# Kernel tuning notes

Measured on AMD Instinct MI355X. Metric: run time of the kernel, lower is better.

The kernel has to match this reference:

```python
import jax, jax.numpy as jnp
import numpy as np

N_SRC = 200000   # source (input) nodes
N_DST = 50000    # destination (output) nodes; dst node i == src node i (block convention)
E = 800000       # edges
IN = 256
OUT = 64
H = 3
SLOPE = 0.2      # leaky_relu negative_slope


def setup_inputs() -> dict:
    key = jax.random.key(0)
    k0, k1, k2, k3, k4, k5 = jax.random.split(key, 6)
    x = jax.random.normal(k0, (N_SRC, IN), dtype=jnp.float32)
    W = jax.random.normal(k1, (H * OUT, IN), dtype=jnp.float32) * (1.0 / np.sqrt(IN))
    attn_l = jax.random.normal(k2, (1, H, OUT), dtype=jnp.float32) * 0.1
    attn_r = jax.random.normal(k3, (1, H, OUT), dtype=jnp.float32) * 0.1
    src = jax.random.randint(k4, (E,), 0, N_SRC, dtype=jnp.int32)
    dst = jnp.sort(jax.random.randint(k5, (E,), 0, N_DST, dtype=jnp.int32))
    return {"x": x, "W": W, "attn_l": attn_l, "attn_r": attn_r, "src": src, "dst": dst}


def reference(x, W, attn_l, attn_r, src, dst):
    # fc + reshape to heads: [N_src, H, F]
    feat = (x @ W.T).reshape(N_SRC, H, OUT)
    # per-head attention logits
    el = jnp.sum(feat * attn_l, axis=-1)          # [N_src, H]
    er = jnp.sum(feat[:N_DST] * attn_r, axis=-1)  # [N_dst, H] (self_gather of out nodes)
    # edge scores: apply_edge + leaky_relu -> [E, H]
    e = jax.nn.leaky_relu(el[src] + er[dst], negative_slope=SLOPE)
    # segmented max over incoming edges of each dst node (gather_local_max)
    m = jax.ops.segment_max(e, dst, num_segments=N_DST)
    m = jnp.where(jnp.isfinite(m), m, jnp.float32(0))  # empty segments -> 0
    m = jax.lax.stop_gradient(m)
    ex = jnp.exp(e - m[dst])                       # [E, H]
    s = jax.ops.segment_sum(ex, dst, num_segments=N_DST)  # [N_dst, H]
    s = jnp.where(s == 0, jnp.float32(1), s)       # sum_exponent[sum==0] = 1
    att = ex / s[dst]                              # [E, H]
    # attention_gather: sum over edges of att * src feature -> [N_dst, H, F]
    out = jax.ops.segment_sum(att[:, :, None] * feat[src], dst, num_segments=N_DST)
    return out.reshape(N_DST, H * OUT)
```

## Files before the change

### kernel.cpp

```cpp
#include <hip/hip_runtime.h>
#include <hip/hip_bf16.h>

#define N_SRCN 200000
#define N_DSTN 50000
#define NEDGE 800000
#define KIN 256
#define NF 192
#define SLOPE 0.2f

typedef __attribute__((ext_vector_type(8))) short bf16x8;
typedef __attribute__((ext_vector_type(4))) float f32x4;

__device__ __forceinline__ unsigned short f2bf(float f) {
    union { float f; unsigned int u; } v; v.f = f;
    unsigned int u = v.u;
    return (unsigned short)((u + 0x7FFFu + ((u >> 16) & 1u)) >> 16);
}
__device__ __forceinline__ float bf2f(unsigned short h) {
    union { unsigned int u; float f; } v; v.u = ((unsigned int)h) << 16;
    return v.f;
}
__device__ __forceinline__ unsigned int cvt2(float lo, float hi) {
    __hip_bfloat162 h = __float22bfloat162_rn(float2{lo, hi});
    union { __hip_bfloat162 h; unsigned int u; } c; c.h = h;
    return c.u;
}

__global__ void prep_kernel(const float* __restrict__ W, unsigned short* __restrict__ Wp,
                            const int* __restrict__ dst, int* __restrict__ rp) {
    const int bid = blockIdx.x;
    if (bid < 24) {
        int tid = bid * 256 + threadIdx.x;
        if (tid >= 12 * 8 * 64) return;
        int lane = tid & 63;
        int g = tid >> 6;
        int nt = g % 12, ks = g / 12;
        int col = nt * 16 + (lane & 15);
        int k = ks * 32 + (lane >> 4) * 8;
        const float* wsrc = &W[col * KIN + k];
        unsigned short* o = &Wp[tid * 8];
        #pragma unroll
        for (int j = 0; j < 8; ++j) o[j] = f2bf(wsrc[j]);
    } else {
        int d = (bid - 24) * 256 + threadIdx.x;
        if (d > N_DSTN) return;
        int lo = 0, hi = NEDGE;
        while (lo < hi) {
            int mid = (lo + hi) >> 1;
            if (dst[mid] < d) lo = mid + 1; else hi = mid;
        }
        rp[d] = lo;
    }
}

__launch_bounds__(64, 4)
__global__ void gemm_feat(const float* __restrict__ x, const unsigned short* __restrict__ Wp,
                          const float* __restrict__ attn_l, const float* __restrict__ attn_r,
                          unsigned short* __restrict__ feat,
                          float* __restrict__ el, float* __restrict__ er) {
    const int lane = threadIdx.x;
    const int al = lane & 15, ah = lane >> 4;
    const int r0 = blockIdx.x * 16;

    const float* xrow = &x[(size_t)(r0 + al) * KIN + ah * 8];

    f32x4 acc[12] = {};
    float4 c0 = *(const float4*)&xrow[0];
    float4 c1 = *(const float4*)&xrow[4];

    #pragma unroll
    for (int ks = 0; ks < 8; ++ks) {
        float4 n0, n1;
        if (ks < 7) {
            n0 = *(const float4*)&xrow[(ks + 1) * 32];
            n1 = *(const float4*)&xrow[(ks + 1) * 32 + 4];
        }
        union { bf16x8 v; unsigned int u[4]; } av;
        av.u[0] = cvt2(c0.x, c0.y);
        av.u[1] = cvt2(c0.z, c0.w);
        av.u[2] = cvt2(c1.x, c1.y);
        av.u[3] = cvt2(c1.z, c1.w);
        const unsigned short* wbase = &Wp[(size_t)(ks * 12) * 512 + lane * 8];
        #pragma unroll
        for (int nt = 0; nt < 12; ++nt) {
            bf16x8 bv = *(const bf16x8*)&wbase[nt * 512];
            acc[nt] = __builtin_amdgcn_mfma_f32_16x16x32_bf16(av.v, bv, acc[nt], 0, 0, 0);
        }
        if (ks < 7) { c0 = n0; c1 = n1; }
    }

    #pragma unroll
    for (int nt = 0; nt < 12; ++nt) {
        const int col = nt * 16 + al;
        #pragma unroll
        for (int e = 0; e < 4; ++e) {
            const int row = r0 + ah * 4 + e;
            feat[(size_t)row * NF + col] = f2bf(acc[nt][e]);
        }
    }

    float Al[12], Ar[12];
    #pragma unroll
    for (int nt = 0; nt < 12; ++nt) {
        Al[nt] = attn_l[nt * 16 + al];
        Ar[nt] = attn_r[nt * 16 + al];
    }
    #pragma unroll
    for (int h = 0; h < 3; ++h) {
        #pragma unroll
        for (int e = 0; e < 4; ++e) {
            float sl = 0.f, sr = 0.f;
            #pragma unroll
            for (int q = 0; q < 4; ++q) {
                const int nt = h * 4 + q;
                sl += acc[nt][e] * Al[nt];
                sr += acc[nt][e] * Ar[nt];
            }
            #pragma unroll
            for (int m = 1; m <= 8; m <<= 1) {
                sl += __shfl_xor(sl, m);
                sr += __shfl_xor(sr, m);
            }
            if (al == 0) {
                const int row = r0 + ah * 4 + e;
                el[row * 3 + h] = sl;
                if (row < N_DSTN) er[row * 3 + h] = sr;
            }
        }
    }
}

__launch_bounds__(256)
__global__ void gather_kernel(const unsigned short* __restrict__ feat,
                              const float* __restrict__ el, const float* __restrict__ er,
                              const int* __restrict__ src, const int* __restrict__ rp,
                              float* __restrict__ out) {
    const int lane = threadIdx.x & 63;
    const int d = (blockIdx.x * blockDim.x + threadIdx.x) >> 6;
    if (d >= N_DSTN) return;
    const int lo = rp[d], hi = rp[d + 1];
    const float er0 = er[d * 3 + 0], er1 = er[d * 3 + 1], er2 = er[d * 3 + 2];

    float a0 = 0.f, a1 = 0.f, a2 = 0.f, s0 = 0.f, s1 = 0.f, s2 = 0.f;
    for (int base = lo; base < hi; base += 64) {
        const int cnt = min(64, hi - base);
        int sv = 0; float w0 = 0.f, w1 = 0.f, w2 = 0.f;
        if (lane < cnt) {
            sv = src[base + lane];
            float e0 = el[sv * 3 + 0] + er0; e0 = e0 >= 0.f ? e0 : SLOPE * e0; w0 = __expf(e0);
            float e1 = el[sv * 3 + 1] + er1; e1 = e1 >= 0.f ? e1 : SLOPE * e1; w1 = __expf(e1);
            float e2 = el[sv * 3 + 2] + er2; e2 = e2 >= 0.f ? e2 : SLOPE * e2; w2 = __expf(e2);
        }
        int j = 0;
        for (; j + 8 <= cnt; j += 8) {
            unsigned short f0[8], f1[8], f2[8];
            float u0[8], u1[8], u2[8];
            #pragma unroll
            for (int q = 0; q < 8; ++q) {
                const int sj = __shfl(sv, j + q);
                const unsigned short* fp = &feat[(size_t)sj * NF + lane];
                f0[q] = fp[0]; f1[q] = fp[64]; f2[q] = fp[128];
                u0[q] = __shfl(w0, j + q);
                u1[q] = __shfl(w1, j + q);
                u2[q] = __shfl(w2, j + q);
            }
            #pragma unroll
            for (int q = 0; q < 8; ++q) {
                s0 += u0[q]; a0 += u0[q] * bf2f(f0[q]);
                s1 += u1[q]; a1 += u1[q] * bf2f(f1[q]);
                s2 += u2[q]; a2 += u2[q] * bf2f(f2[q]);
            }
        }
        for (; j < cnt; ++j) {
            const int sj = __shfl(sv, j);
            const float u0 = __shfl(w0, j);
            const float u1 = __shfl(w1, j);
            const float u2 = __shfl(w2, j);
            const unsigned short* fp = &feat[(size_t)sj * NF + lane];
            s0 += u0; a0 += u0 * bf2f(fp[0]);
            s1 += u1; a1 += u1 * bf2f(fp[64]);
            s2 += u2; a2 += u2 * bf2f(fp[128]);
        }
    }
    if (hi == lo) { s0 = 1.f; s1 = 1.f; s2 = 1.f; }
    float* op = &out[(size_t)d * NF];
    op[lane]       = a0 / s0;
    op[64 + lane]  = a1 / s1;
    op[128 + lane] = a2 / s2;
}

extern "C" void kernel_launch(void* const* d_in, const int* in_sizes, int n_in,
                              void* d_out, int out_size, void* d_ws, size_t ws_size,
                              hipStream_t stream) {
    const float* x      = (const float*)d_in[0];
    const float* W      = (const float*)d_in[1];
    const float* attn_l = (const float*)d_in[2];
    const float* attn_r = (const float*)d_in[3];
    const int*   src    = (const int*)d_in[4];
    const int*   dst    = (const int*)d_in[5];
    float* out = (float*)d_out;

    char* ws = (char*)d_ws;
    unsigned short* feat = (unsigned short*)ws;
    float* el = (float*)(ws + 76800000);
    float* er = (float*)(ws + 79200000);
    unsigned short* Wp = (unsigned short*)(ws + 79800000);
    int*   rp = (int*)(ws + 79898304);

    prep_kernel<<<24 + 196, 256, 0, stream>>>(W, Wp, dst, rp);
    gemm_feat<<<12500, 64, 0, stream>>>(x, Wp, attn_l, attn_r, feat, el, er);
    gather_kernel<<<12500, 256, 0, stream>>>(feat, el, er, src, rp, out);
}
```

Before: 180.1 us.

## Make GEMM persistent with LDS-staged weights and pad el/er to float4

The feature GEMM becomes a persistent kernel of 256 blocks of 8 waves. Each block loads the packed bf16 weight matrix into LDS once with direct global-to-LDS loads, then loops over 16-row tiles, so the weights are no longer re-read from global memory for every tile. The el/er logits are stored with a stride of 4 floats so the gather kernel can fetch them with a single float4 load. In exchange, the software prefetch of x across k-steps is dropped, occupancy is limited to one 512-thread block per CU, and the el/er buffers become larger.

```diff
diff --git a/kernel.cpp b/kernel.cpp
--- a/kernel.cpp
+++ b/kernel.cpp
@@ -7,6 +7,8 @@
 #define KIN 256
 #define NF 192
 #define SLOPE 0.2f
+#define TILES16 12500
+#define NWAVES 2048
 
 typedef __attribute__((ext_vector_type(8))) short bf16x8;
 typedef __attribute__((ext_vector_type(4))) float f32x4;
@@ -24,6 +26,11 @@
     __hip_bfloat162 h = __float22bfloat162_rn(float2{lo, hi});
     union { __hip_bfloat162 h; unsigned int u; } c; c.h = h;
     return c.u;
+}
+__device__ __forceinline__ void gl_lds16(const void* g, void* l) {
+    __builtin_amdgcn_global_load_lds(
+        (const __attribute__((address_space(1))) unsigned int*)g,
+        (__attribute__((address_space(3))) unsigned int*)l, 16, 0, 0);
 }
 
 __global__ void prep_kernel(const float* __restrict__ W, unsigned short* __restrict__ Wp,
@@ -53,51 +60,23 @@
     }
 }
 
-__launch_bounds__(64, 4)
-__global__ void gemm_feat(const float* __restrict__ x, const unsigned short* __restrict__ Wp,
-                          const float* __restrict__ attn_l, const float* __restrict__ attn_r,
-                          unsigned short* __restrict__ feat,
-                          float* __restrict__ el, float* __restrict__ er) {
-    const int lane = threadIdx.x;
+__global__ void __launch_bounds__(512, 1)
+gemm_feat(const float* __restrict__ x, const unsigned short* __restrict__ Wp,
+          const float* __restrict__ attn_l, const float* __restrict__ attn_r,
+          unsigned short* __restrict__ feat,
+          float* __restrict__ el4, float* __restrict__ er4) {
+    __shared__ unsigned short Bl[12 * 8 * 512];
+    const int t = threadIdx.x;
+    const int wid = t >> 6, lane = t & 63;
     const int al = lane & 15, ah = lane >> 4;
-    const int r0 = blockIdx.x * 16;
-
-    const float* xrow = &x[(size_t)(r0 + al) * KIN + ah * 8];
-
-    f32x4 acc[12] = {};
-    float4 c0 = *(const float4*)&xrow[0];
-    float4 c1 = *(const float4*)&xrow[4];
 
     #pragma unroll
-    for (int ks = 0; ks < 8; ++ks) {
-        float4 n0, n1;
-        if (ks < 7) {
-            n0 = *(const float4*)&xrow[(ks + 1) * 32];
-            n1 = *(const float4*)&xrow[(ks + 1) * 32 + 4];
-        }
-        union { bf16x8 v; unsigned int u[4]; } av;
-        av.u[0] = cvt2(c0.x, c0.y);
-        av.u[1] = cvt2(c0.z, c0.w);
-        av.u[2] = cvt2(c1.x, c1.y);
-        av.u[3] = cvt2(c1.z, c1.w);
-        const unsigned short* wbase = &Wp[(size_t)(ks * 12) * 512 + lane * 8];
-        #pragma unroll
-        for (int nt = 0; nt < 12; ++nt) {
-            bf16x8 bv = *(const bf16x8*)&wbase[nt * 512];
-            acc[nt] = __builtin_amdgcn_mfma_f32_16x16x32_bf16(av.v, bv, acc[nt], 0, 0, 0);
-        }
-        if (ks < 7) { c0 = n0; c1 = n1; }
-    }
-
-    #pragma unroll
-    for (int nt = 0; nt < 12; ++nt) {
-        const int col = nt * 16 + al;
-        #pragma unroll
-        for (int e = 0; e < 4; ++e) {
-            const int row = r0 + ah * 4 + e;
-            feat[(size_t)row * NF + col] = f2bf(acc[nt][e]);
-        }
-    }
+    for (int i = 0; i < 12; ++i) {
+        const int off = (i * 8 + wid) * 1024;
+        gl_lds16((const char*)Wp + off + lane * 16, (char*)Bl + off);
+    }
+    asm volatile("s_waitcnt vmcnt(0)" ::: "memory");
+    __syncthreads();
 
     float Al[12], Ar[12];
     #pragma unroll
@@ -105,26 +84,60 @@
         Al[nt] = attn_l[nt * 16 + al];
         Ar[nt] = attn_r[nt * 16 + al];
     }
-    #pragma unroll
-    for (int h = 0; h < 3; ++h) {
-        #pragma unroll
-        for (int e = 0; e < 4; ++e) {
-            float sl = 0.f, sr = 0.f;
-            #pragma unroll
-            for (int q = 0; q < 4; ++q) {
-                const int nt = h * 4 + q;
-                sl += acc[nt][e] * Al[nt];
-                sr += acc[nt][e] * Ar[nt];
-            }
-            #pragma unroll
-            for (int m = 1; m <= 8; m <<= 1) {
-                sl += __shfl_xor(sl, m);
-                sr += __shfl_xor(sr, m);
-            }
-            if (al == 0) {
+
+    const int gw = blockIdx.x * 8 + wid;
+    for (int tile = gw; tile < TILES16; tile += NWAVES) {
+        const int r0 = tile * 16;
+        const float* xrow = &x[(size_t)(r0 + al) * KIN + ah * 8];
+
+        f32x4 acc[12] = {};
+        #pragma unroll
+        for (int ks = 0; ks < 8; ++ks) {
+            const float4 a0 = *(const float4*)&xrow[ks * 32];
+            const float4 a1 = *(const float4*)&xrow[ks * 32 + 4];
+            union { bf16x8 v; unsigned int u[4]; } av;
+            av.u[0] = cvt2(a0.x, a0.y);
+            av.u[1] = cvt2(a0.z, a0.w);
+            av.u[2] = cvt2(a1.x, a1.y);
+            av.u[3] = cvt2(a1.z, a1.w);
+            #pragma unroll
+            for (int nt = 0; nt < 12; ++nt) {
+                const bf16x8 bv = *(const bf16x8*)&Bl[(ks * 12 + nt) * 512 + lane * 8];
+                acc[nt] = __builtin_amdgcn_mfma_f32_16x16x32_bf16(av.v, bv, acc[nt], 0, 0, 0);
+            }
+        }
+
+        #pragma unroll
+        for (int nt = 0; nt < 12; ++nt) {
+            const int col = nt * 16 + al;
+            #pragma unroll
+            for (int e = 0; e < 4; ++e) {
                 const int row = r0 + ah * 4 + e;
-                el[row * 3 + h] = sl;
-                if (row < N_DSTN) er[row * 3 + h] = sr;
+                feat[(size_t)row * NF + col] = f2bf(acc[nt][e]);
+            }
+        }
+
+        #pragma unroll
+        for (int h = 0; h < 3; ++h) {
+            #pragma unroll
+            for (int e = 0; e < 4; ++e) {
+                float sl = 0.f, sr = 0.f;
+                #pragma unroll
+                for (int q = 0; q < 4; ++q) {
+                    const int nt = h * 4 + q;
+                    sl += acc[nt][e] * Al[nt];
+                    sr += acc[nt][e] * Ar[nt];
+                }
+                #pragma unroll
+                for (int m = 1; m <= 8; m <<= 1) {
+                    sl += __shfl_xor(sl, m);
+                    sr += __shfl_xor(sr, m);
+                }
+                if (al == 0) {
+                    const int row = r0 + ah * 4 + e;
+                    el4[(size_t)row * 4 + h] = sl;
+                    if (row < N_DSTN) er4[(size_t)row * 4 + h] = sr;
+                }
             }
         }
     }
@@ -132,14 +145,14 @@
 
 __launch_bounds__(256)
 __global__ void gather_kernel(const unsigned short* __restrict__ feat,
-                              const float* __restrict__ el, const float* __restrict__ er,
+                              const float* __restrict__ el4, const float* __restrict__ er4,
                               const int* __restrict__ src, const int* __restrict__ rp,
                               float* __restrict__ out) {
     const int lane = threadIdx.x & 63;
     const int d = (blockIdx.x * blockDim.x + threadIdx.x) >> 6;
     if (d >= N_DSTN) return;
     const int lo = rp[d], hi = rp[d + 1];
-    const float er0 = er[d * 3 + 0], er1 = er[d * 3 + 1], er2 = er[d * 3 + 2];
+    const float4 erv = *(const float4*)&er4[(size_t)d * 4];
 
     float a0 = 0.f, a1 = 0.f, a2 = 0.f, s0 = 0.f, s1 = 0.f, s2 = 0.f;
     for (int base = lo; base < hi; base += 64) {
@@ -147,9 +160,10 @@
         int sv = 0; float w0 = 0.f, w1 = 0.f, w2 = 0.f;
         if (lane < cnt) {
             sv = src[base + lane];
-            float e0 = el[sv * 3 + 0] + er0; e0 = e0 >= 0.f ? e0 : SLOPE * e0; w0 = __expf(e0);
-            float e1 = el[sv * 3 + 1] + er1; e1 = e1 >= 0.f ? e1 : SLOPE * e1; w1 = __expf(e1);
-            float e2 = el[sv * 3 + 2] + er2; e2 = e2 >= 0.f ? e2 : SLOPE * e2; w2 = __expf(e2);
+            const float4 elv = *(const float4*)&el4[(size_t)sv * 4];
+            float e0 = elv.x + erv.x; e0 = e0 >= 0.f ? e0 : SLOPE * e0; w0 = __expf(e0);
+            float e1 = elv.y + erv.y; e1 = e1 >= 0.f ? e1 : SLOPE * e1; w1 = __expf(e1);
+            float e2 = elv.z + erv.z; e2 = e2 >= 0.f ? e2 : SLOPE * e2; w2 = __expf(e2);
         }
         int j = 0;
         for (; j + 8 <= cnt; j += 8) {
@@ -202,12 +216,12 @@
 
     char* ws = (char*)d_ws;
     unsigned short* feat = (unsigned short*)ws;
-    float* el = (float*)(ws + 76800000);
-    float* er = (float*)(ws + 79200000);
-    unsigned short* Wp = (unsigned short*)(ws + 79800000);
-    int*   rp = (int*)(ws + 79898304);
+    float* el4 = (float*)(ws + 76800000);
+    float* er4 = (float*)(ws + 80000000);
+    unsigned short* Wp = (unsigned short*)(ws + 80800000);
+    int*   rp = (int*)(ws + 80898304);
 
     prep_kernel<<<24 + 196, 256, 0, stream>>>(W, Wp, dst, rp);
-    gemm_feat<<<12500, 64, 0, stream>>>(x, Wp, attn_l, attn_r, feat, el, er);
-    gather_kernel<<<12500, 256, 0, stream>>>(feat, el, er, src, rp, out);
-}
+    gemm_feat<<<256, 512, 0, stream>>>(x, Wp, attn_l, attn_r, feat, el4, er4);
+    gather_kernel<<<12500, 256, 0, stream>>>(feat, el4, er4, src, rp, out);
+}
```

Result: faster. 149.8 us (-16.8%).
